# Performance work log

Hardware: AMD Instinct MI355X
Metric: run time of the kernel (lower is better)

The kernel has to match this reference:

```python
import jax, jax.numpy as jnp
import numpy as np
import math

D_MODEL = 1024
NUM_HEADS = 16
D_HEAD = 64
K_EIG = 16
B, N = 4, 4096


def setup_inputs() -> dict:
    key = jax.random.key(0)
    ks = jax.random.split(key, 8)
    s = 1.0 / math.sqrt(D_MODEL)
    return {
        "x": jax.random.normal(ks[0], (B, N, D_MODEL), jnp.float32),
        "Wq": jax.random.normal(ks[1], (D_MODEL, NUM_HEADS * D_HEAD), jnp.float32) * s,
        "bq": jnp.zeros((NUM_HEADS * D_HEAD,), jnp.float32),
        "Wk": jax.random.normal(ks[2], (D_MODEL, NUM_HEADS * D_HEAD), jnp.float32) * s,
        "bk": jnp.zeros((NUM_HEADS * D_HEAD,), jnp.float32),
        "Wv": jax.random.normal(ks[3], (D_MODEL, NUM_HEADS * D_HEAD), jnp.float32) * s,
        "bv": jnp.zeros((NUM_HEADS * D_HEAD,), jnp.float32),
        "eigenvectors": jax.random.normal(ks[4], (NUM_HEADS, K_EIG), jnp.float32),
        "filter_weights": jnp.ones((K_EIG,), jnp.float32),
    }


def reference(x, Wq, bq, Wk, bk, Wv, bv, eigenvectors, filter_weights):
    Bb, Nn, _ = x.shape
    H, Dh = NUM_HEADS, D_HEAD
    # projections -> [B,N,H,Dh]
    Q = (x @ Wq + bq).reshape(Bb, Nn, H, Dh)
    K = (x @ Wk + bk).reshape(Bb, Nn, H, Dh)
    V = (x @ Wv + bv).reshape(Bb, Nn, H, Dh)
    # head axis -> eigen (frequency) axis: [B,N,K,Dh]
    Qf = jnp.einsum('hk,bnhd->bnkd', eigenvectors, Q)
    Kf = jnp.einsum('hk,bnhd->bnkd', eigenvectors, K)
    Vf = jnp.einsum('hk,bnhd->bnkd', eigenvectors, V)
    # learnable spectral filter, broadcast over eigen axis
    w = filter_weights[None, None, :, None]
    Qf = Qf * w
    Kf = Kf * w
    Vf = Vf * w
    # small k x k attention per token
    scores = jnp.einsum('bnkd,bnld->bnkl', Qf, Kf) / math.sqrt(Dh)
    attn = jax.nn.softmax(scores, axis=-1)  # dropout is identity in eval
    out_f = jnp.einsum('bnkl,bnld->bnkd', attn, Vf)
    # back to head space: [B,N,H,Dh]
    out = jnp.einsum('hk,bnkd->bnhd', eigenvectors, out_f)
    return out.reshape(Bb, Nn, H * Dh)
```

## Files before the change

### kernel.cpp

```cpp
#include <hip/hip_runtime.h>
#include <stdint.h>

#define NTOK   16384
#define DM     1024
#define NQKV   3072

typedef __attribute__((ext_vector_type(8))) _Float16 half8;
typedef __attribute__((ext_vector_type(4))) _Float16 half4;
typedef __attribute__((ext_vector_type(4))) float    float4v;

__device__ __forceinline__ void async_cp16(const void* g, void* l){
  __builtin_amdgcn_global_load_lds(
      (const __attribute__((address_space(1))) void*)g,
      (__attribute__((address_space(3))) void*)l, 16, 0, 0);
}

__global__ void cvt_x_kernel(const float* __restrict__ x, _Float16* __restrict__ xb){
  int i = (blockIdx.x * blockDim.x + threadIdx.x) * 4;
  const int stride = gridDim.x * blockDim.x * 4;
  for(; i < NTOK * DM; i += stride){
    float4v v = *(const float4v*)(x + i);
    half4 o;
    o[0]=(_Float16)v[0]; o[1]=(_Float16)v[1]; o[2]=(_Float16)v[2]; o[3]=(_Float16)v[3];
    *(half4*)(xb + i) = o;
  }
}

__global__ void prep_w_kernel(const float* __restrict__ Wq, const float* __restrict__ Wk,
                              const float* __restrict__ Wv, const float* __restrict__ E,
                              const float* __restrict__ fw, _Float16* __restrict__ WT){
  const int nt = blockIdx.x;
  const int p  = nt >> 4, kE = nt & 15;
  const int c0 = blockIdx.y * 64;
  const float* W = (p == 0) ? Wq : (p == 1) ? Wk : Wv;
  __shared__ _Float16 tile[64][66];
  __shared__ float Ecol[16];
  const int t = threadIdx.x;
  if(t < 16) Ecol[t] = E[t * 16 + kE];
  __syncthreads();
  const float wk = fw[kE];
  const int d = t & 63, cw = t >> 6;
  for(int pass = 0; pass < 16; ++pass){
    const int cl = pass * 4 + cw;
    const float* row = W + (c0 + cl) * 1024 + d;
    float acc = 0.f;
    #pragma unroll
    for(int h = 0; h < 16; ++h) acc += Ecol[h] * row[h * 64];
    tile[d][cl] = (_Float16)(acc * wk);
  }
  __syncthreads();
  const int d2 = t >> 2, cb = (t & 3) * 16;
  _Float16* dst = WT + (size_t)(nt * 64 + d2) * 1024 + c0 + cb;
  #pragma unroll
  for(int j = 0; j < 16; ++j) dst[j] = tile[d2][cb + j];
}

__global__ void prep_b_kernel(const float* __restrict__ bq, const float* __restrict__ bk,
                              const float* __restrict__ bv, const float* __restrict__ E,
                              const float* __restrict__ fw, float* __restrict__ fb){
  const int n = blockIdx.x * blockDim.x + threadIdx.x;
  if(n >= NQKV) return;
  const int p = n >> 10, kE = (n >> 6) & 15, d = n & 63;
  const float* b = (p == 0) ? bq : (p == 1) ? bk : bv;
  float acc = 0.f;
  for(int h = 0; h < 16; ++h) acc += E[h * 16 + kE] * b[h * 64 + d];
  fb[n] = acc * fw[kE];
}

__global__ __launch_bounds__(256)
void gemm_qkv_kernel(const _Float16* __restrict__ A,
                     const _Float16* __restrict__ BT,
                     const float* __restrict__ bias,
                     _Float16* __restrict__ C){
  __shared__ _Float16 As[128 * 32];
  __shared__ _Float16 Bs[128 * 32];
  const int t = threadIdx.x;
  const int lane = t & 63, wv = t >> 6;
  const int l15 = lane & 15, q = lane >> 4;
  const int m0 = blockIdx.y * 128, n0 = blockIdx.x * 128;
  const int wm = (wv & 1) * 64, wn = (wv >> 1) * 64;

  float4v acc[4][4];
  #pragma unroll
  for(int i = 0; i < 4; ++i)
    #pragma unroll
    for(int j = 0; j < 4; ++j){ acc[i][j][0]=0.f; acc[i][j][1]=0.f; acc[i][j][2]=0.f; acc[i][j][3]=0.f; }

  const int ar = t >> 2;
  const int ac = (t & 3) * 8;
  const _Float16* ga0 = A  + (size_t)(m0 + ar)      * 1024 + ac;
  const _Float16* ga1 = A  + (size_t)(m0 + 64 + ar) * 1024 + ac;
  const _Float16* gb0 = BT + (size_t)(n0 + ar)      * 1024 + ac;
  const _Float16* gb1 = BT + (size_t)(n0 + 64 + ar) * 1024 + ac;

  for(int k0 = 0; k0 < 1024; k0 += 32){
    async_cp16(ga0 + k0, As + t * 8);
    async_cp16(ga1 + k0, As + 2048 + t * 8);
    async_cp16(gb0 + k0, Bs + t * 8);
    async_cp16(gb1 + k0, Bs + 2048 + t * 8);
    __syncthreads();
    half8 af[4], bf[4];
    #pragma unroll
    for(int i = 0; i < 4; ++i) af[i] = *(const half8*)(As + (wm + i * 16 + l15) * 32 + q * 8);
    #pragma unroll
    for(int j = 0; j < 4; ++j) bf[j] = *(const half8*)(Bs + (wn + j * 16 + l15) * 32 + q * 8);
    #pragma unroll
    for(int i = 0; i < 4; ++i)
      #pragma unroll
      for(int j = 0; j < 4; ++j)
        acc[i][j] = __builtin_amdgcn_mfma_f32_16x16x32_f16(af[i], bf[j], acc[i][j], 0, 0, 0);
    __syncthreads();
  }
  #pragma unroll
  for(int j = 0; j < 4; ++j){
    const int n = n0 + wn + j * 16 + l15;
    const float bs = bias[n];
    #pragma unroll
    for(int i = 0; i < 4; ++i){
      const int mg = m0 + wm + i * 16 + q * 4;
      #pragma unroll
      for(int r = 0; r < 4; ++r)
        C[(size_t)(mg + r) * NQKV + n] = (_Float16)(acc[i][j][r] + bs);
    }
  }
}

__global__ __launch_bounds__(256)
void attn_kernel(const _Float16* __restrict__ QKV,
                 const float* __restrict__ E,
                 float* __restrict__ out){
  const int t = threadIdx.x;
  const int lane = t & 63, wv = t >> 6;
  const int tok = blockIdx.x * 4 + wv;
  const int l15 = lane & 15, q = lane >> 4;
  __shared__ float Gs[4][16][20];

  const _Float16* base = QKV + (size_t)tok * NQKV;

  half8 aq0 = *(const half8*)(base + l15 * 64 + q * 8);
  half8 aq1 = *(const half8*)(base + l15 * 64 + 32 + q * 8);
  half8 bk0 = *(const half8*)(base + 1024 + l15 * 64 + q * 8);
  half8 bk1 = *(const half8*)(base + 1024 + l15 * 64 + 32 + q * 8);
  float4v S; S[0]=0.f; S[1]=0.f; S[2]=0.f; S[3]=0.f;
  S = __builtin_amdgcn_mfma_f32_16x16x32_f16(aq0, bk0, S, 0, 0, 0);
  S = __builtin_amdgcn_mfma_f32_16x16x32_f16(aq1, bk1, S, 0, 0, 0);

  float p[4];
  #pragma unroll
  for(int r = 0; r < 4; ++r){
    float v = S[r] * 0.125f;
    float mx = v;
    #pragma unroll
    for(int m = 1; m < 16; m <<= 1) mx = fmaxf(mx, __shfl_xor(mx, m));
    float e = __expf(v - mx);
    float sm = e;
    #pragma unroll
    for(int m = 1; m < 16; m <<= 1) sm += __shfl_xor(sm, m);
    p[r] = e / sm;
  }

  half8 pfrag;
  #pragma unroll
  for(int jj = 0; jj < 8; ++jj){
    const int k = q * 8 + jj;
    const int srcLane = ((k >> 2) & 3) * 16 + l15;
    float val = __shfl(p[jj & 3], srcLane, 64);
    if(q >= 2) val = 0.f;
    pfrag[jj] = (_Float16)val;
  }

  half8 efrag;
  #pragma unroll
  for(int jj = 0; jj < 8; ++jj){
    const int k = q * 8 + jj;
    float ev = (q < 2) ? E[l15 * 16 + (k & 15)] : 0.f;
    efrag[jj] = (_Float16)ev;
  }
  float4v G; G[0]=0.f; G[1]=0.f; G[2]=0.f; G[3]=0.f;
  G = __builtin_amdgcn_mfma_f32_16x16x32_f16(efrag, pfrag, G, 0, 0, 0);

  #pragma unroll
  for(int r = 0; r < 4; ++r) Gs[wv][q * 4 + r][l15] = G[r];
  const int off = (q < 2) ? q * 8 : 0;
  float4v g0 = *(const float4v*)&Gs[wv][l15][off];
  float4v g1 = *(const float4v*)&Gs[wv][l15][off + 4];
  half8 gfrag;
  #pragma unroll
  for(int jj = 0; jj < 4; ++jj){
    gfrag[jj]     = (q < 2) ? (_Float16)g0[jj] : (_Float16)0.f;
    gfrag[jj + 4] = (q < 2) ? (_Float16)g1[jj] : (_Float16)0.f;
  }

  #pragma unroll
  for(int tt = 0; tt < 4; ++tt){
    half8 vfrag;
    #pragma unroll
    for(int jj = 0; jj < 8; ++jj){
      const int k = q * 8 + jj;
      vfrag[jj] = (q < 2) ? base[2048 + (k & 15) * 64 + tt * 16 + l15] : (_Float16)0.f;
    }
    float4v O; O[0]=0.f; O[1]=0.f; O[2]=0.f; O[3]=0.f;
    O = __builtin_amdgcn_mfma_f32_16x16x32_f16(gfrag, vfrag, O, 0, 0, 0);
    #pragma unroll
    for(int r = 0; r < 4; ++r)
      out[(size_t)tok * 1024 + (q * 4 + r) * 64 + tt * 16 + l15] = O[r];
  }
}

extern "C" void kernel_launch(void* const* d_in, const int* in_sizes, int n_in,
                              void* d_out, int out_size, void* d_ws, size_t ws_size,
                              hipStream_t stream){
  const float* x  = (const float*)d_in[0];
  const float* Wq = (const float*)d_in[1];
  const float* bq = (const float*)d_in[2];
  const float* Wk = (const float*)d_in[3];
  const float* bk = (const float*)d_in[4];
  const float* Wv = (const float*)d_in[5];
  const float* bv = (const float*)d_in[6];
  const float* E  = (const float*)d_in[7];
  const float* fw = (const float*)d_in[8];
  float* out = (float*)d_out;

  char* ws = (char*)d_ws;
  _Float16* xb  = (_Float16*)ws;
  _Float16* WT  = (_Float16*)(ws + (size_t)32 * 1024 * 1024);
  float*    fb  = (float*)   (ws + (size_t)39 * 1024 * 1024);
  _Float16* QKV = (_Float16*)(ws + (size_t)40 * 1024 * 1024);

  hipLaunchKernelGGL(cvt_x_kernel, dim3(4096), dim3(256), 0, stream, x, xb);
  hipLaunchKernelGGL(prep_w_kernel, dim3(48, 16), dim3(256), 0, stream, Wq, Wk, Wv, E, fw, WT);
  hipLaunchKernelGGL(prep_b_kernel, dim3(12), dim3(256), 0, stream, bq, bk, bv, E, fw, fb);
  hipLaunchKernelGGL(gemm_qkv_kernel, dim3(24, 128), dim3(256), 0, stream, xb, WT, fb, QKV);
  hipLaunchKernelGGL(attn_kernel, dim3(NTOK / 4), dim3(256), 0, stream, QKV, E, out);
}
```

Baseline: 324.4 us.

## Stage per-token QKV in LDS for attention and retile weight-prep kernel

The attention kernel now copies each block's four tokens of Q/K/V into shared memory with async global-to-LDS loads and builds the MFMA fragments from LDS. Scores are computed transposed (K times Q), so the softmax reduction needs only two cross-lane shuffles. Probability and mixing matrices are passed through small zero-padded LDS tiles instead of per-element shuffles and global reads of E. The weight-prep kernel is restructured to stage W tiles in LDS with coalesced reads, and each thread accumulates four eigen outputs. The cost is more LDS per block, which may lower occupancy in the attention kernel.

```diff
diff --git a/kernel.cpp b/kernel.cpp
--- a/kernel.cpp
+++ b/kernel.cpp
@@ -26,33 +26,54 @@
   }
 }
 
-__global__ void prep_w_kernel(const float* __restrict__ Wq, const float* __restrict__ Wk,
-                              const float* __restrict__ Wv, const float* __restrict__ E,
-                              const float* __restrict__ fw, _Float16* __restrict__ WT){
-  const int nt = blockIdx.x;
-  const int p  = nt >> 4, kE = nt & 15;
-  const int c0 = blockIdx.y * 64;
+__global__ __launch_bounds__(256)
+void prep_w_kernel(const float* __restrict__ Wq, const float* __restrict__ Wk,
+                   const float* __restrict__ Wv, const float* __restrict__ E,
+                   const float* __restrict__ fw, _Float16* __restrict__ WT){
+  __shared__ float Wl[64][65];
+  __shared__ float sEv[256];
+  const int t  = threadIdx.x;
+  const int bx = blockIdx.x;
+  const int p  = bx >> 6, kg = (bx >> 4) & 3, ct = bx & 15;
   const float* W = (p == 0) ? Wq : (p == 1) ? Wk : Wv;
-  __shared__ _Float16 tile[64][66];
-  __shared__ float Ecol[16];
-  const int t = threadIdx.x;
-  if(t < 16) Ecol[t] = E[t * 16 + kE];
-  __syncthreads();
-  const float wk = fw[kE];
-  const int d = t & 63, cw = t >> 6;
-  for(int pass = 0; pass < 16; ++pass){
-    const int cl = pass * 4 + cw;
-    const float* row = W + (c0 + cl) * 1024 + d;
-    float acc = 0.f;
-    #pragma unroll
-    for(int h = 0; h < 16; ++h) acc += Ecol[h] * row[h * 64];
-    tile[d][cl] = (_Float16)(acc * wk);
-  }
-  __syncthreads();
-  const int d2 = t >> 2, cb = (t & 3) * 16;
-  _Float16* dst = WT + (size_t)(nt * 64 + d2) * 1024 + c0 + cb;
-  #pragma unroll
-  for(int j = 0; j < 16; ++j) dst[j] = tile[d2][cb + j];
+  sEv[t] = E[t];
+  const int c_l = t & 63, dg = t >> 6;
+  const int c0 = ct * 64;
+  float acc[4][16];
+  #pragma unroll
+  for(int ke = 0; ke < 4; ++ke)
+    #pragma unroll
+    for(int i = 0; i < 16; ++i) acc[ke][i] = 0.f;
+
+  for(int h = 0; h < 16; ++h){
+    __syncthreads();
+    #pragma unroll
+    for(int j = 0; j < 16; ++j){
+      const int flat = j * 256 + t;
+      const int rowc = flat >> 6, cold = flat & 63;
+      Wl[rowc][cold] = W[(size_t)(c0 + rowc) * 1024 + h * 64 + cold];
+    }
+    __syncthreads();
+    float ew[4];
+    #pragma unroll
+    for(int ke = 0; ke < 4; ++ke) ew[ke] = sEv[h * 16 + kg * 4 + ke];
+    #pragma unroll
+    for(int i = 0; i < 16; ++i){
+      const float w = Wl[c_l][dg * 16 + i];
+      #pragma unroll
+      for(int ke = 0; ke < 4; ++ke) acc[ke][i] += ew[ke] * w;
+    }
+  }
+  #pragma unroll
+  for(int ke = 0; ke < 4; ++ke){
+    const int kE = kg * 4 + ke;
+    const float s = fw[kE];
+    #pragma unroll
+    for(int i = 0; i < 16; ++i){
+      const int n = (p * 16 + kE) * 64 + dg * 16 + i;
+      WT[(size_t)n * 1024 + c0 + c_l] = (_Float16)(acc[ke][i] * s);
+    }
+  }
 }
 
 __global__ void prep_b_kernel(const float* __restrict__ bq, const float* __restrict__ bk,
@@ -129,81 +150,87 @@
 void attn_kernel(const _Float16* __restrict__ QKV,
                  const float* __restrict__ E,
                  float* __restrict__ out){
-  const int t = threadIdx.x;
-  const int lane = t & 63, wv = t >> 6;
+  __shared__ _Float16 sQ[4 * 3072];
+  __shared__ _Float16 sE[16 * 32];
+  __shared__ _Float16 pT[4][16 * 32];
+  __shared__ _Float16 gT[4][16 * 32];
+
+  const int t = threadIdx.x, lane = t & 63, wv = t >> 6;
+  const int l15 = lane & 15, q = lane >> 4;
+
+  {
+    #pragma unroll
+    for(int s = 0; s < 2; ++s){
+      const int idx = s * 256 + t;
+      const int row = idx >> 5, col = idx & 31;
+      sE[idx] = (col < 16) ? (_Float16)E[row * 16 + col] : (_Float16)0.f;
+    }
+    #pragma unroll
+    for(int s = 0; s < 4; ++s){
+      const int idx = s * 256 + t;
+      const int w = idx >> 8, rem = idx & 255;
+      const int off = (rem >> 4) * 32 + 16 + (rem & 15);
+      pT[w][off] = (_Float16)0.f;
+      gT[w][off] = (_Float16)0.f;
+    }
+  }
+
+  const _Float16* gb = QKV + (size_t)blockIdx.x * (4 * 3072);
+  #pragma unroll
+  for(int i = 0; i < 6; ++i) async_cp16(gb + (i * 256 + t) * 8, sQ + (i * 256 + t) * 8);
+  __syncthreads();
+
   const int tok = blockIdx.x * 4 + wv;
-  const int l15 = lane & 15, q = lane >> 4;
-  __shared__ float Gs[4][16][20];
-
-  const _Float16* base = QKV + (size_t)tok * NQKV;
-
-  half8 aq0 = *(const half8*)(base + l15 * 64 + q * 8);
-  half8 aq1 = *(const half8*)(base + l15 * 64 + 32 + q * 8);
-  half8 bk0 = *(const half8*)(base + 1024 + l15 * 64 + q * 8);
-  half8 bk1 = *(const half8*)(base + 1024 + l15 * 64 + 32 + q * 8);
+  const _Float16* tb = sQ + wv * 3072;
+
+  half8 aK0 = *(const half8*)(tb + 1024 + l15 * 64 + q * 8);
+  half8 aK1 = *(const half8*)(tb + 1024 + l15 * 64 + 32 + q * 8);
+  half8 bQ0 = *(const half8*)(tb + l15 * 64 + q * 8);
+  half8 bQ1 = *(const half8*)(tb + l15 * 64 + 32 + q * 8);
   float4v S; S[0]=0.f; S[1]=0.f; S[2]=0.f; S[3]=0.f;
-  S = __builtin_amdgcn_mfma_f32_16x16x32_f16(aq0, bk0, S, 0, 0, 0);
-  S = __builtin_amdgcn_mfma_f32_16x16x32_f16(aq1, bk1, S, 0, 0, 0);
-
-  float p[4];
-  #pragma unroll
-  for(int r = 0; r < 4; ++r){
-    float v = S[r] * 0.125f;
-    float mx = v;
-    #pragma unroll
-    for(int m = 1; m < 16; m <<= 1) mx = fmaxf(mx, __shfl_xor(mx, m));
-    float e = __expf(v - mx);
-    float sm = e;
-    #pragma unroll
-    for(int m = 1; m < 16; m <<= 1) sm += __shfl_xor(sm, m);
-    p[r] = e / sm;
-  }
-
-  half8 pfrag;
-  #pragma unroll
-  for(int jj = 0; jj < 8; ++jj){
-    const int k = q * 8 + jj;
-    const int srcLane = ((k >> 2) & 3) * 16 + l15;
-    float val = __shfl(p[jj & 3], srcLane, 64);
-    if(q >= 2) val = 0.f;
-    pfrag[jj] = (_Float16)val;
-  }
-
-  half8 efrag;
-  #pragma unroll
-  for(int jj = 0; jj < 8; ++jj){
-    const int k = q * 8 + jj;
-    float ev = (q < 2) ? E[l15 * 16 + (k & 15)] : 0.f;
-    efrag[jj] = (_Float16)ev;
-  }
+  S = __builtin_amdgcn_mfma_f32_16x16x32_f16(aK0, bQ0, S, 0, 0, 0);
+  S = __builtin_amdgcn_mfma_f32_16x16x32_f16(aK1, bQ1, S, 0, 0, 0);
+
+  float v[4];
+  #pragma unroll
+  for(int r = 0; r < 4; ++r) v[r] = S[r] * 0.125f;
+  float mx = fmaxf(fmaxf(v[0], v[1]), fmaxf(v[2], v[3]));
+  mx = fmaxf(mx, __shfl_xor(mx, 16));
+  mx = fmaxf(mx, __shfl_xor(mx, 32));
+  float e[4];
+  #pragma unroll
+  for(int r = 0; r < 4; ++r) e[r] = __expf(v[r] - mx);
+  float sm = (e[0] + e[1]) + (e[2] + e[3]);
+  sm += __shfl_xor(sm, 16);
+  sm += __shfl_xor(sm, 32);
+  const float rs = 1.f / sm;
+
+  _Float16* pw = pT[wv];
+  #pragma unroll
+  for(int r = 0; r < 4; ++r) pw[(q * 4 + r) * 32 + l15] = (_Float16)(e[r] * rs);
+  half8 bP = *(const half8*)(pw + l15 * 32 + q * 8);
+  half8 aE = *(const half8*)(sE + l15 * 32 + q * 8);
+
   float4v G; G[0]=0.f; G[1]=0.f; G[2]=0.f; G[3]=0.f;
-  G = __builtin_amdgcn_mfma_f32_16x16x32_f16(efrag, pfrag, G, 0, 0, 0);
-
-  #pragma unroll
-  for(int r = 0; r < 4; ++r) Gs[wv][q * 4 + r][l15] = G[r];
-  const int off = (q < 2) ? q * 8 : 0;
-  float4v g0 = *(const float4v*)&Gs[wv][l15][off];
-  float4v g1 = *(const float4v*)&Gs[wv][l15][off + 4];
-  half8 gfrag;
-  #pragma unroll
-  for(int jj = 0; jj < 4; ++jj){
-    gfrag[jj]     = (q < 2) ? (_Float16)g0[jj] : (_Float16)0.f;
-    gfrag[jj + 4] = (q < 2) ? (_Float16)g1[jj] : (_Float16)0.f;
-  }
-
+  G = __builtin_amdgcn_mfma_f32_16x16x32_f16(aE, bP, G, 0, 0, 0);
+
+  _Float16* gw = gT[wv];
+  #pragma unroll
+  for(int r = 0; r < 4; ++r) gw[(q * 4 + r) * 32 + l15] = (_Float16)G[r];
+  half8 aG = *(const half8*)(gw + l15 * 32 + q * 8);
+
+  const _Float16* vb = tb + 2048 + (q & 1) * 8 * 64;
+  float* ob = out + (size_t)tok * 1024;
   #pragma unroll
   for(int tt = 0; tt < 4; ++tt){
-    half8 vfrag;
-    #pragma unroll
-    for(int jj = 0; jj < 8; ++jj){
-      const int k = q * 8 + jj;
-      vfrag[jj] = (q < 2) ? base[2048 + (k & 15) * 64 + tt * 16 + l15] : (_Float16)0.f;
-    }
+    half8 vf;
+    #pragma unroll
+    for(int jj = 0; jj < 8; ++jj) vf[jj] = vb[jj * 64 + tt * 16 + l15];
     float4v O; O[0]=0.f; O[1]=0.f; O[2]=0.f; O[3]=0.f;
-    O = __builtin_amdgcn_mfma_f32_16x16x32_f16(gfrag, vfrag, O, 0, 0, 0);
+    O = __builtin_amdgcn_mfma_f32_16x16x32_f16(aG, vf, O, 0, 0, 0);
     #pragma unroll
     for(int r = 0; r < 4; ++r)
-      out[(size_t)tok * 1024 + (q * 4 + r) * 64 + tt * 16 + l15] = O[r];
+      ob[(q * 4 + r) * 64 + tt * 16 + l15] = O[r];
   }
 }
 
@@ -228,7 +255,7 @@
   _Float16* QKV = (_Float16*)(ws + (size_t)40 * 1024 * 1024);
 
   hipLaunchKernelGGL(cvt_x_kernel, dim3(4096), dim3(256), 0, stream, x, xb);
-  hipLaunchKernelGGL(prep_w_kernel, dim3(48, 16), dim3(256), 0, stream, Wq, Wk, Wv, E, fw, WT);
+  hipLaunchKernelGGL(prep_w_kernel, dim3(192), dim3(256), 0, stream, Wq, Wk, Wv, E, fw, WT);
   hipLaunchKernelGGL(prep_b_kernel, dim3(12), dim3(256), 0, stream, bq, bk, bv, E, fw, fb);
   hipLaunchKernelGGL(gemm_qkv_kernel, dim3(24, 128), dim3(256), 0, stream, xb, WT, fb, QKV);
   hipLaunchKernelGGL(attn_kernel, dim3(NTOK / 4), dim3(256), 0, stream, QKV, E, out);
```

New measurement: 411.3 us. 26.8% more time.
